# Performance work log

Measured on AMD Instinct MI355X. Metric: run time of the kernel, lower is better.

Reference implementation:

```python
import jax, jax.numpy as jnp
import numpy as np

B, T = 16384, 512          # batch, seq_len
DSTATE, DINPUT = 4, 4       # quaternion state / quaternion input
DMLP1, DMLP2 = 128, 128     # ODEFunc MLP hidden widths


def _linear_params(key, fan_in, fan_out):
    # torch nn.Linear default init: U(-1/sqrt(fan_in), 1/sqrt(fan_in))
    lim = 1.0 / np.sqrt(fan_in)
    kw, kb = jax.random.split(key)
    W = jax.random.uniform(kw, (fan_in, fan_out), jnp.float32, -lim, lim)
    b = jax.random.uniform(kb, (fan_out,), jnp.float32, -lim, lim)
    return W, b


def setup_inputs() -> dict:
    key = jax.random.key(0)
    k1, k2, k3, kx = jax.random.split(key, 4)
    W1, b1 = _linear_params(k1, DSTATE + DINPUT, DMLP1)
    W2, b2 = _linear_params(k2, DMLP1, DMLP2)
    W3, b3 = _linear_params(k3, DMLP2, DSTATE)
    quat_seq = jax.random.normal(kx, (B, T, DINPUT), jnp.float32)
    return {"quat_seq": quat_seq, "W1": W1, "b1": b1, "W2": W2, "b2": b2,
            "W3": W3, "b3": b3}


def reference(quat_seq, W1, b1, W2, b2, W3, b3):
    batch = quat_seq.shape[0]
    dstate = W3.shape[1]

    def odefunc(h, q):
        # f(t, [h, q]) -> dh/dt ; time is unused by the net
        x = jnp.concatenate([h, q], axis=-1)            # [B, DSTATE+DINPUT]
        x = jax.nn.silu(x @ W1 + b1)                    # [B, DMLP1]
        x = jax.nn.silu(x @ W2 + b2)                    # [B, DMLP2]
        return x @ W3 + b3                              # [B, DSTATE]

    dt = 1.0  # t_span = [0, 1] on a fixed grid -> single RK4 step of size 1

    def step(h, q_t):
        # torchdiffeq fixed-grid 'rk4' uses the 3/8-rule (rk4_alt_step_func)
        k1 = odefunc(h, q_t)
        k2 = odefunc(h + dt * k1 / 3.0, q_t)
        k3 = odefunc(h + dt * (k2 - k1 / 3.0), q_t)
        k4 = odefunc(h + dt * (k1 - k2 + k3), q_t)
        h_new = h + dt * (k1 + 3.0 * (k2 + k3) + k4) / 8.0
        return h_new, None

    h0 = jnp.zeros((batch, dstate), quat_seq.dtype).at[:, 0].set(1.0)
    # scan over time: [T, B, DINPUT]
    h_final, _ = jax.lax.scan(step, h0, jnp.swapaxes(quat_seq, 0, 1))
    return h_final
```

## Files before the change

kernel.cpp:

```cpp
#include <hip/hip_runtime.h>
#include <hip/hip_bf16.h>

typedef float f32x4 __attribute__((ext_vector_type(4)));
typedef short short8v __attribute__((ext_vector_type(8)));
typedef unsigned int uint;

constexpr int TSTEPS = 512;

union FragU { uint u[4]; short8v v; };

__device__ __forceinline__ float silu_f(float x) {
    return __fdividef(x, 1.0f + __expf(-x));
}

__device__ __forceinline__ uint bf16_rne(float x) {
    uint ux = __float_as_uint(x);
    return (ux + 0x7FFFu + ((ux >> 16) & 1u)) & 0xFFFF0000u;
}
__device__ __forceinline__ void split2u(float x, uint &h, uint &l) {
    h = bf16_rne(x);
    float rem = x - __uint_as_float(h);
    l = bf16_rne(rem);
}

__device__ __forceinline__ uint cvtpk(float a, float b) {
    union { __hip_bfloat162 h; uint u; } cv;
    cv.h = __float22bfloat162_rn(make_float2(a, b));
    return cv.u;
}
__device__ __forceinline__ void split4_pk(const f32x4 v, uint2 &hi, uint2 &lo) {
    hi.x = cvtpk(v.x, v.y);
    hi.y = cvtpk(v.z, v.w);
    float h0 = __uint_as_float(hi.x << 16);
    float h1 = __uint_as_float(hi.x & 0xFFFF0000u);
    float h2 = __uint_as_float(hi.y << 16);
    float h3 = __uint_as_float(hi.y & 0xFFFF0000u);
    lo.x = cvtpk(v.x - h0, v.y - h1);
    lo.y = cvtpk(v.z - h2, v.w - h3);
}

__device__ __forceinline__ f32x4 mfma4(const short8v *A, short8v Bh, short8v Bl,
                                       f32x4 c) {
    c = __builtin_amdgcn_mfma_f32_16x16x32_bf16(A[1], Bl, c, 0, 0, 0);
    c = __builtin_amdgcn_mfma_f32_16x16x32_bf16(A[1], Bh, c, 0, 0, 0);
    c = __builtin_amdgcn_mfma_f32_16x16x32_bf16(A[0], Bl, c, 0, 0, 0);
    c = __builtin_amdgcn_mfma_f32_16x16x32_bf16(A[0], Bh, c, 0, 0, 0);
    return c;
}

__global__ __launch_bounds__(256, 3)
void odernn_v7(const float* __restrict__ quat,
               const float* __restrict__ W1, const float* __restrict__ b1,
               const float* __restrict__ W2, const float* __restrict__ b2,
               const float* __restrict__ W3, const float* __restrict__ b3,
               float* __restrict__ out)
{
    __shared__ short sx1[2 * 16 * 16 * 8];
    __shared__ float sb1[128];
    __shared__ float sb2[128];
    __shared__ float sW3[128 * 4];
    __shared__ float sk3[4][16][4];

    const int tid  = threadIdx.x;
    const int w    = tid >> 6;
    const int lane = tid & 63;
    const int l15  = lane & 15;
    const int g    = lane >> 4;
    const int rowbase = blockIdx.x * 16;

    if (tid < 128) { sb1[tid] = b1[tid]; sb2[tid] = b2[tid]; }
    for (int i = tid; i < 512; i += 256) sW3[i] = W3[i];

    short8v A2[2][4][2];
#pragma unroll
    for (int mt = 0; mt < 2; ++mt) {
#pragma unroll
        for (int kt = 0; kt < 4; ++kt) {
#pragma unroll
            for (int e = 0; e < 8; ++e) {
                float x = W2[(32 * kt + 8 * g + e) * 128 + (32 * w + 16 * mt + l15)];
                uint h, l; split2u(x, h, l);
                A2[mt][kt][0][e] = (short)(h >> 16);
                A2[mt][kt][1][e] = (short)(l >> 16);
            }
        }
    }
    short8v A1[2];
#pragma unroll
    for (int mt = 0; mt < 2; ++mt) {
#pragma unroll
        for (int e = 0; e < 8; ++e) {
            float x = W1[e * 128 + (32 * w + 16 * mt + l15)];
            uint h, l; split2u(x, h, l);
            A1[mt][e] = (short)(((g < 2) ? h : l) >> 16);
        }
    }
    f32x4 b3v = *(const f32x4*)b3;

    __syncthreads();

    f32x4 h  = {1.0f, 0, 0, 0};
    f32x4 k1 = {0,0,0,0}, k2 = {0,0,0,0}, k3v = {0,0,0,0};
    const float* qp = quat + (size_t)(rowbase + l15) * TSTEPS * 4;

    const bool gsel = (g & 1);
    const int  half = (g & 1) * 4;
    const int  kc0  = 4 * w + (g >> 1);

#pragma unroll 1
    for (int t = 0; t < TSTEPS; ++t) {
        f32x4 q = *(const f32x4*)(qp + 4 * t);
        uint qs01, qs23;
        {
            uint2 qhi, qlo;
            split4_pk(q, qhi, qlo);
            qs01 = gsel ? qlo.x : qhi.x;
            qs23 = gsel ? qlo.y : qhi.y;
        }
        f32x4 hnew = {0,0,0,0};

#pragma unroll
        for (int s = 0; s < 4; ++s) {
            f32x4 hs = h;
            if (s == 1)      hs += k1 * (1.0f/3.0f);
            else if (s == 2) hs += k2 - k1 * (1.0f/3.0f);
            else if (s == 3) hs += k1 - k2 + k3v;

            FragU b0;
            {
                uint2 hhi, hlo;
                split4_pk(hs, hhi, hlo);
                b0.u[0] = gsel ? hlo.x : hhi.x;
                b0.u[1] = gsel ? hlo.y : hhi.y;
                b0.u[2] = qs01;
                b0.u[3] = qs23;
            }

            f32x4 c1_0 = *(const f32x4*)&sb1[32 * w + 4 * g];
            f32x4 c1_1 = *(const f32x4*)&sb1[32 * w + 16 + 4 * g];
            c1_0 = __builtin_amdgcn_mfma_f32_16x16x32_bf16(A1[0], b0.v, c1_0, 0, 0, 0);
            c1_1 = __builtin_amdgcn_mfma_f32_16x16x32_bf16(A1[1], b0.v, c1_1, 0, 0, 0);

#pragma unroll
            for (int mt = 0; mt < 2; ++mt) {
                const f32x4 c1 = mt ? c1_1 : c1_0;
                f32x4 sv;
#pragma unroll
                for (int r = 0; r < 4; ++r) sv[r] = silu_f(c1[r]);
                uint2 phi, plo;
                split4_pk(sv, phi, plo);
                const int kc = kc0 + 2 * mt;
                *(uint2*)&sx1[((0 * 16 + kc) * 16 + l15) * 8 + half] = phi;
                *(uint2*)&sx1[((1 * 16 + kc) * 16 + l15) * 8 + half] = plo;
            }
            __syncthreads();

            f32x4 u0 = *(const f32x4*)&sb2[32 * w + 4 * g],      v0 = {0,0,0,0};
            f32x4 u1 = *(const f32x4*)&sb2[32 * w + 16 + 4 * g], v1 = {0,0,0,0};
#pragma unroll
            for (int kt = 0; kt < 4; ++kt) {
                short8v Bh = *(const short8v*)&sx1[((0 * 16 + kt * 4 + g) * 16 + l15) * 8];
                short8v Bl = *(const short8v*)&sx1[((1 * 16 + kt * 4 + g) * 16 + l15) * 8];
                if (kt & 1) {
                    v0 = mfma4(A2[0][kt], Bh, Bl, v0);
                    v1 = mfma4(A2[1][kt], Bh, Bl, v1);
                } else {
                    u0 = mfma4(A2[0][kt], Bh, Bl, u0);
                    u1 = mfma4(A2[1][kt], Bh, Bl, u1);
                }
            }
            const f32x4 c20 = u0 + v0, c21 = u1 + v1;

            f32x4 p = {0,0,0,0};
#pragma unroll
            for (int mt = 0; mt < 2; ++mt) {
#pragma unroll
                for (int r = 0; r < 4; ++r) {
                    const int j = 32 * w + 16 * mt + 4 * g + r;
                    const float xv = silu_f(mt ? c21[r] : c20[r]);
                    p += xv * (*(const f32x4*)&sW3[j * 4]);
                }
            }
#pragma unroll
            for (int mx = 16; mx < 64; mx <<= 1) {
                p.x += __shfl_xor(p.x, mx, 64);
                p.y += __shfl_xor(p.y, mx, 64);
                p.z += __shfl_xor(p.z, mx, 64);
                p.w += __shfl_xor(p.w, mx, 64);
            }
            if (g == 0) *(f32x4*)&sk3[w][l15][0] = p;
            __syncthreads();

            f32x4 ks = b3v;
#pragma unroll
            for (int w2 = 0; w2 < 4; ++w2)
                ks += *(const f32x4*)&sk3[w2][l15][0];

            const float wgt = (s == 1 || s == 2) ? 0.375f : 0.125f;
            hnew += ks * wgt;
            if (s == 0)      k1  = ks;
            else if (s == 1) k2  = ks;
            else if (s == 2) k3v = ks;
        }
        h += hnew;
    }

    if (tid < 16)
        *(f32x4*)&out[(size_t)(rowbase + tid) * 4] = h;
}

extern "C" void kernel_launch(void* const* d_in, const int* in_sizes, int n_in,
                              void* d_out, int out_size, void* d_ws, size_t ws_size,
                              hipStream_t stream)
{
    const float* quat = (const float*)d_in[0];
    const float* W1   = (const float*)d_in[1];
    const float* b1   = (const float*)d_in[2];
    const float* W2   = (const float*)d_in[3];
    const float* b2   = (const float*)d_in[4];
    const float* W3   = (const float*)d_in[5];
    const float* b3   = (const float*)d_in[6];
    float* out        = (float*)d_out;

    const int B = in_sizes[0] / (TSTEPS * 4);
    dim3 grid(B / 16), block(256);
    hipLaunchKernelGGL(odernn_v7, grid, block, 0, stream,
                       quat, W1, b1, W2, b2, W3, b3, out);
}
```

Before: 7.830 ms.

## Switch to 32x32x16 MFMA tiles with 32 batch rows per block

Each block now handles 32 batch rows instead of 16 and uses 32x32x16 bf16 MFMAs in place of 16x16x32 ones for both MLP layers, with the shared-memory staging layout redone to match. This halves the grid and the per-row barrier and bias overhead, and puts more work into each MFMA issue. In exchange each block carries more accumulator registers, so launch bounds drop to 2 blocks per SM. The layer-1 split-bf16 trick becomes two MFMAs that swap the hi/lo halves.

Measured after the change: 7.385 ms. 5.7% less time.

```diff
diff --git a/kernel.cpp b/kernel.cpp
--- a/kernel.cpp
+++ b/kernel.cpp
@@ -1,7 +1,8 @@
 #include <hip/hip_runtime.h>
 #include <hip/hip_bf16.h>
 
-typedef float f32x4 __attribute__((ext_vector_type(4)));
+typedef float f32x4  __attribute__((ext_vector_type(4)));
+typedef float f32x16 __attribute__((ext_vector_type(16)));
 typedef short short8v __attribute__((ext_vector_type(8)));
 typedef unsigned int uint;
 
@@ -39,61 +40,48 @@
     lo.y = cvtpk(v.z - h2, v.w - h3);
 }
 
-__device__ __forceinline__ f32x4 mfma4(const short8v *A, short8v Bh, short8v Bl,
-                                       f32x4 c) {
-    c = __builtin_amdgcn_mfma_f32_16x16x32_bf16(A[1], Bl, c, 0, 0, 0);
-    c = __builtin_amdgcn_mfma_f32_16x16x32_bf16(A[1], Bh, c, 0, 0, 0);
-    c = __builtin_amdgcn_mfma_f32_16x16x32_bf16(A[0], Bl, c, 0, 0, 0);
-    c = __builtin_amdgcn_mfma_f32_16x16x32_bf16(A[0], Bh, c, 0, 0, 0);
-    return c;
-}
-
-__global__ __launch_bounds__(256, 3)
-void odernn_v7(const float* __restrict__ quat,
+#define SX1(lev,kt,gk,b) (((((lev)*8+(kt))*2+(gk))*32+(b))*8)
+
+__global__ __launch_bounds__(256, 2)
+void odernn_v8(const float* __restrict__ quat,
                const float* __restrict__ W1, const float* __restrict__ b1,
                const float* __restrict__ W2, const float* __restrict__ b2,
                const float* __restrict__ W3, const float* __restrict__ b3,
                float* __restrict__ out)
 {
-    __shared__ short sx1[2 * 16 * 16 * 8];
+    __shared__ short sx1[2 * 8 * 2 * 32 * 8];
     __shared__ float sb1[128];
     __shared__ float sb2[128];
-    __shared__ float sW3[128 * 4];
-    __shared__ float sk3[4][16][4];
+    __shared__ float sW3[512];
+    __shared__ float sk3[4][32][4];
 
     const int tid  = threadIdx.x;
     const int w    = tid >> 6;
     const int lane = tid & 63;
-    const int l15  = lane & 15;
-    const int g    = lane >> 4;
-    const int rowbase = blockIdx.x * 16;
+    const int b    = lane & 31;
+    const int gp   = lane >> 5;
+    const int rowbase = blockIdx.x * 32;
 
     if (tid < 128) { sb1[tid] = b1[tid]; sb2[tid] = b2[tid]; }
     for (int i = tid; i < 512; i += 256) sW3[i] = W3[i];
 
-    short8v A2[2][4][2];
-#pragma unroll
-    for (int mt = 0; mt < 2; ++mt) {
-#pragma unroll
-        for (int kt = 0; kt < 4; ++kt) {
-#pragma unroll
-            for (int e = 0; e < 8; ++e) {
-                float x = W2[(32 * kt + 8 * g + e) * 128 + (32 * w + 16 * mt + l15)];
-                uint h, l; split2u(x, h, l);
-                A2[mt][kt][0][e] = (short)(h >> 16);
-                A2[mt][kt][1][e] = (short)(l >> 16);
-            }
+    short8v A2[8][2];
+#pragma unroll
+    for (int kt = 0; kt < 8; ++kt) {
+#pragma unroll
+        for (int e = 0; e < 8; ++e) {
+            float x = W2[(16 * kt + 8 * gp + e) * 128 + (32 * w + b)];
+            uint h, l; split2u(x, h, l);
+            A2[kt][0][e] = (short)(h >> 16);
+            A2[kt][1][e] = (short)(l >> 16);
         }
     }
-    short8v A1[2];
-#pragma unroll
-    for (int mt = 0; mt < 2; ++mt) {
-#pragma unroll
-        for (int e = 0; e < 8; ++e) {
-            float x = W1[e * 128 + (32 * w + 16 * mt + l15)];
-            uint h, l; split2u(x, h, l);
-            A1[mt][e] = (short)(((g < 2) ? h : l) >> 16);
-        }
+    short8v A1;
+#pragma unroll
+    for (int e = 0; e < 8; ++e) {
+        float x = W1[e * 128 + (32 * w + b)];
+        uint h, l; split2u(x, h, l);
+        A1[e] = (short)((gp ? l : h) >> 16);
     }
     f32x4 b3v = *(const f32x4*)b3;
 
@@ -101,22 +89,13 @@
 
     f32x4 h  = {1.0f, 0, 0, 0};
     f32x4 k1 = {0,0,0,0}, k2 = {0,0,0,0}, k3v = {0,0,0,0};
-    const float* qp = quat + (size_t)(rowbase + l15) * TSTEPS * 4;
-
-    const bool gsel = (g & 1);
-    const int  half = (g & 1) * 4;
-    const int  kc0  = 4 * w + (g >> 1);
+    const float* qp = quat + (size_t)(rowbase + b) * TSTEPS * 4;
 
 #pragma unroll 1
     for (int t = 0; t < TSTEPS; ++t) {
         f32x4 q = *(const f32x4*)(qp + 4 * t);
-        uint qs01, qs23;
-        {
-            uint2 qhi, qlo;
-            split4_pk(q, qhi, qlo);
-            qs01 = gsel ? qlo.x : qhi.x;
-            qs23 = gsel ? qlo.y : qhi.y;
-        }
+        uint2 qhi, qlo;
+        split4_pk(q, qhi, qlo);
         f32x4 hnew = {0,0,0,0};
 
 #pragma unroll
@@ -126,75 +105,73 @@
             else if (s == 2) hs += k2 - k1 * (1.0f/3.0f);
             else if (s == 3) hs += k1 - k2 + k3v;
 
-            FragU b0;
-            {
-                uint2 hhi, hlo;
-                split4_pk(hs, hhi, hlo);
-                b0.u[0] = gsel ? hlo.x : hhi.x;
-                b0.u[1] = gsel ? hlo.y : hhi.y;
-                b0.u[2] = qs01;
-                b0.u[3] = qs23;
-            }
-
-            f32x4 c1_0 = *(const f32x4*)&sb1[32 * w + 4 * g];
-            f32x4 c1_1 = *(const f32x4*)&sb1[32 * w + 16 + 4 * g];
-            c1_0 = __builtin_amdgcn_mfma_f32_16x16x32_bf16(A1[0], b0.v, c1_0, 0, 0, 0);
-            c1_1 = __builtin_amdgcn_mfma_f32_16x16x32_bf16(A1[1], b0.v, c1_1, 0, 0, 0);
-
-#pragma unroll
-            for (int mt = 0; mt < 2; ++mt) {
-                const f32x4 c1 = mt ? c1_1 : c1_0;
+            uint2 hhi, hlo;
+            split4_pk(hs, hhi, hlo);
+            FragU b0a, b0b;
+            b0a.u[0] = gp ? hlo.x : hhi.x;  b0a.u[1] = gp ? hlo.y : hhi.y;
+            b0a.u[2] = gp ? qlo.x : qhi.x;  b0a.u[3] = gp ? qlo.y : qhi.y;
+            b0b.u[0] = gp ? hhi.x : hlo.x;  b0b.u[1] = gp ? hhi.y : hlo.y;
+            b0b.u[2] = gp ? qhi.x : qlo.x;  b0b.u[3] = gp ? qhi.y : qlo.y;
+
+            f32x16 c1;
+#pragma unroll
+            for (int qd = 0; qd < 4; ++qd) {
+                f32x4 bv = *(const f32x4*)&sb1[32 * w + 8 * qd + 4 * gp];
+                c1[4*qd+0] = bv.x; c1[4*qd+1] = bv.y;
+                c1[4*qd+2] = bv.z; c1[4*qd+3] = bv.w;
+            }
+            c1 = __builtin_amdgcn_mfma_f32_32x32x16_bf16(A1, b0a.v, c1, 0, 0, 0);
+            c1 = __builtin_amdgcn_mfma_f32_32x32x16_bf16(A1, b0b.v, c1, 0, 0, 0);
+
+#pragma unroll
+            for (int qd = 0; qd < 4; ++qd) {
                 f32x4 sv;
-#pragma unroll
-                for (int r = 0; r < 4; ++r) sv[r] = silu_f(c1[r]);
+                sv.x = silu_f(c1[4*qd+0]); sv.y = silu_f(c1[4*qd+1]);
+                sv.z = silu_f(c1[4*qd+2]); sv.w = silu_f(c1[4*qd+3]);
                 uint2 phi, plo;
                 split4_pk(sv, phi, plo);
-                const int kc = kc0 + 2 * mt;
-                *(uint2*)&sx1[((0 * 16 + kc) * 16 + l15) * 8 + half] = phi;
-                *(uint2*)&sx1[((1 * 16 + kc) * 16 + l15) * 8 + half] = plo;
+                const int kt = 2 * w + (qd >> 1);
+                const int gk = qd & 1;
+                *(uint2*)&sx1[SX1(0, kt, gk, b) + 4 * gp] = phi;
+                *(uint2*)&sx1[SX1(1, kt, gk, b) + 4 * gp] = plo;
             }
             __syncthreads();
 
-            f32x4 u0 = *(const f32x4*)&sb2[32 * w + 4 * g],      v0 = {0,0,0,0};
-            f32x4 u1 = *(const f32x4*)&sb2[32 * w + 16 + 4 * g], v1 = {0,0,0,0};
-#pragma unroll
-            for (int kt = 0; kt < 4; ++kt) {
-                short8v Bh = *(const short8v*)&sx1[((0 * 16 + kt * 4 + g) * 16 + l15) * 8];
-                short8v Bl = *(const short8v*)&sx1[((1 * 16 + kt * 4 + g) * 16 + l15) * 8];
-                if (kt & 1) {
-                    v0 = mfma4(A2[0][kt], Bh, Bl, v0);
-                    v1 = mfma4(A2[1][kt], Bh, Bl, v1);
-                } else {
-                    u0 = mfma4(A2[0][kt], Bh, Bl, u0);
-                    u1 = mfma4(A2[1][kt], Bh, Bl, u1);
-                }
-            }
-            const f32x4 c20 = u0 + v0, c21 = u1 + v1;
+            f32x16 c2;
+#pragma unroll
+            for (int qd = 0; qd < 4; ++qd) {
+                f32x4 bv = *(const f32x4*)&sb2[32 * w + 8 * qd + 4 * gp];
+                c2[4*qd+0] = bv.x; c2[4*qd+1] = bv.y;
+                c2[4*qd+2] = bv.z; c2[4*qd+3] = bv.w;
+            }
+#pragma unroll
+            for (int kt = 0; kt < 8; ++kt) {
+                short8v Bh = *(const short8v*)&sx1[SX1(0, kt, gp, b)];
+                short8v Bl = *(const short8v*)&sx1[SX1(1, kt, gp, b)];
+                c2 = __builtin_amdgcn_mfma_f32_32x32x16_bf16(A2[kt][1], Bl, c2, 0, 0, 0);
+                c2 = __builtin_amdgcn_mfma_f32_32x32x16_bf16(A2[kt][1], Bh, c2, 0, 0, 0);
+                c2 = __builtin_amdgcn_mfma_f32_32x32x16_bf16(A2[kt][0], Bl, c2, 0, 0, 0);
+                c2 = __builtin_amdgcn_mfma_f32_32x32x16_bf16(A2[kt][0], Bh, c2, 0, 0, 0);
+            }
 
             f32x4 p = {0,0,0,0};
 #pragma unroll
-            for (int mt = 0; mt < 2; ++mt) {
-#pragma unroll
-                for (int r = 0; r < 4; ++r) {
-                    const int j = 32 * w + 16 * mt + 4 * g + r;
-                    const float xv = silu_f(mt ? c21[r] : c20[r]);
-                    p += xv * (*(const f32x4*)&sW3[j * 4]);
-                }
-            }
-#pragma unroll
-            for (int mx = 16; mx < 64; mx <<= 1) {
-                p.x += __shfl_xor(p.x, mx, 64);
-                p.y += __shfl_xor(p.y, mx, 64);
-                p.z += __shfl_xor(p.z, mx, 64);
-                p.w += __shfl_xor(p.w, mx, 64);
-            }
-            if (g == 0) *(f32x4*)&sk3[w][l15][0] = p;
+            for (int i = 0; i < 16; ++i) {
+                const int j = 32 * w + 8 * (i >> 2) + (i & 3) + 4 * gp;
+                const float xv = silu_f(c2[i]);
+                p += xv * (*(const f32x4*)&sW3[j * 4]);
+            }
+            p.x += __shfl_xor(p.x, 32, 64);
+            p.y += __shfl_xor(p.y, 32, 64);
+            p.z += __shfl_xor(p.z, 32, 64);
+            p.w += __shfl_xor(p.w, 32, 64);
+            if (lane < 32) *(f32x4*)&sk3[w][lane][0] = p;
             __syncthreads();
 
             f32x4 ks = b3v;
 #pragma unroll
             for (int w2 = 0; w2 < 4; ++w2)
-                ks += *(const f32x4*)&sk3[w2][l15][0];
+                ks += *(const f32x4*)&sk3[w2][b][0];
 
             const float wgt = (s == 1 || s == 2) ? 0.375f : 0.125f;
             hnew += ks * wgt;
@@ -205,7 +182,7 @@
         h += hnew;
     }
 
-    if (tid < 16)
+    if (tid < 32)
         *(f32x4*)&out[(size_t)(rowbase + tid) * 4] = h;
 }
 
@@ -223,7 +200,7 @@
     float* out        = (float*)d_out;
 
     const int B = in_sizes[0] / (TSTEPS * 4);
-    dim3 grid(B / 16), block(256);
-    hipLaunchKernelGGL(odernn_v7, grid, block, 0, stream,
+    dim3 grid(B / 32), block(256);
+    hipLaunchKernelGGL(odernn_v8, grid, block, 0, stream,
                        quat, W1, b1, W2, b2, W3, b3, out);
 }
```

## Run each 16-row tile in a single wavefront, removing block barriers

Applied to the files above, without the earlier changes.

Each 16-row batch tile now runs in one 64-thread wavefront instead of four waves. The wave keeps all of W2 (hi/lo bf16 split) in registers, folds b1 into the layer-1 MFMA through a constant-one input lane, and computes layer 3 with MFMAs instead of a shuffle reduction. This removes the per-stage __syncthreads and the cross-wave reduction, drops one of the four bf16 split products in layer 2, and prefetches the next quaternion. In exchange it puts a large register footprint on each wave and gives up intra-block parallelism, so latency hiding depends on having enough resident blocks.

Result: slower. 9.457 ms (+20.8%).

```diff
diff --git a/kernel.cpp b/kernel.cpp
--- a/kernel.cpp
+++ b/kernel.cpp
@@ -11,6 +11,12 @@
 
 __device__ __forceinline__ float silu_f(float x) {
     return __fdividef(x, 1.0f + __expf(-x));
+}
+__device__ __forceinline__ f32x4 silu4(f32x4 v) {
+    f32x4 r;
+    r.x = silu_f(v.x); r.y = silu_f(v.y);
+    r.z = silu_f(v.z); r.w = silu_f(v.w);
+    return r;
 }
 
 __device__ __forceinline__ uint bf16_rne(float x) {
@@ -22,7 +28,6 @@
     float rem = x - __uint_as_float(h);
     l = bf16_rne(rem);
 }
-
 __device__ __forceinline__ uint cvtpk(float a, float b) {
     union { __hip_bfloat162 h; uint u; } cv;
     cv.h = __float22bfloat162_rn(make_float2(a, b));
@@ -39,84 +44,85 @@
     lo.y = cvtpk(v.z - h2, v.w - h3);
 }
 
-__device__ __forceinline__ f32x4 mfma4(const short8v *A, short8v Bh, short8v Bl,
-                                       f32x4 c) {
-    c = __builtin_amdgcn_mfma_f32_16x16x32_bf16(A[1], Bl, c, 0, 0, 0);
-    c = __builtin_amdgcn_mfma_f32_16x16x32_bf16(A[1], Bh, c, 0, 0, 0);
-    c = __builtin_amdgcn_mfma_f32_16x16x32_bf16(A[0], Bl, c, 0, 0, 0);
-    c = __builtin_amdgcn_mfma_f32_16x16x32_bf16(A[0], Bh, c, 0, 0, 0);
-    return c;
-}
-
-__global__ __launch_bounds__(256, 3)
-void odernn_v7(const float* __restrict__ quat,
-               const float* __restrict__ W1, const float* __restrict__ b1,
-               const float* __restrict__ W2, const float* __restrict__ b2,
-               const float* __restrict__ W3, const float* __restrict__ b3,
-               float* __restrict__ out)
+#define MFMA16(A, B, C) __builtin_amdgcn_mfma_f32_16x16x32_bf16((A), (B), (C), 0, 0, 0)
+
+#define SXI(lev, p, bb) ((((lev)*16 + (p))*16 + (bb))*8)
+
+__global__ __launch_bounds__(64, 1)
+void odernn_v11(const float* __restrict__ quat,
+                const float* __restrict__ W1, const float* __restrict__ b1,
+                const float* __restrict__ W2, const float* __restrict__ b2,
+                const float* __restrict__ W3, const float* __restrict__ b3,
+                float* __restrict__ out)
 {
     __shared__ short sx1[2 * 16 * 16 * 8];
-    __shared__ float sb1[128];
-    __shared__ float sb2[128];
-    __shared__ float sW3[128 * 4];
-    __shared__ float sk3[4][16][4];
-
-    const int tid  = threadIdx.x;
-    const int w    = tid >> 6;
-    const int lane = tid & 63;
-    const int l15  = lane & 15;
-    const int g    = lane >> 4;
+    __shared__ short sx2[2 * 16 * 16 * 8];
+    __shared__ float sb2s[128];
+    __shared__ float sck[64];
+
+    const int tid = threadIdx.x;
+    const int b   = tid & 15;
+    const int g   = tid >> 4;
     const int rowbase = blockIdx.x * 16;
 
-    if (tid < 128) { sb1[tid] = b1[tid]; sb2[tid] = b2[tid]; }
-    for (int i = tid; i < 512; i += 256) sW3[i] = W3[i];
-
-    short8v A2[2][4][2];
-#pragma unroll
-    for (int mt = 0; mt < 2; ++mt) {
-#pragma unroll
-        for (int kt = 0; kt < 4; ++kt) {
+    sb2s[tid]      = b2[tid];
+    sb2s[tid + 64] = b2[tid + 64];
+
+    short8v A2[8][4][2];
+#pragma unroll
+    for (int jt = 0; jt < 8; ++jt)
+#pragma unroll
+        for (int kt = 0; kt < 4; ++kt)
 #pragma unroll
             for (int e = 0; e < 8; ++e) {
-                float x = W2[(32 * kt + 8 * g + e) * 128 + (32 * w + 16 * mt + l15)];
-                uint h, l; split2u(x, h, l);
-                A2[mt][kt][0][e] = (short)(h >> 16);
-                A2[mt][kt][1][e] = (short)(l >> 16);
-            }
+                uint h_, l_;
+                split2u(W2[(32*kt + 8*g + e) * 128 + (16*jt + b)], h_, l_);
+                A2[jt][kt][0][e] = (short)(h_ >> 16);
+                A2[jt][kt][1][e] = (short)(l_ >> 16);
+            }
+
+    short8v A1[8];
+#pragma unroll
+    for (int jt = 0; jt < 8; ++jt)
+#pragma unroll
+        for (int e = 0; e < 8; ++e) {
+            short val;
+            if (g == 3) {
+                uint h_, l_; split2u(b1[16*jt + b], h_, l_);
+                val = (e == 0) ? (short)(h_ >> 16) : (e == 1) ? (short)(l_ >> 16) : (short)0;
+            } else {
+                uint h_, l_; split2u(W1[e * 128 + 16*jt + b], h_, l_);
+                val = (short)(((g == 2) ? l_ : h_) >> 16);
+            }
+            A1[jt][e] = val;
         }
-    }
-    short8v A1[2];
-#pragma unroll
-    for (int mt = 0; mt < 2; ++mt) {
+
+    short8v A3[4][2];
+#pragma unroll
+    for (int kt = 0; kt < 4; ++kt)
 #pragma unroll
         for (int e = 0; e < 8; ++e) {
-            float x = W1[e * 128 + (32 * w + 16 * mt + l15)];
-            uint h, l; split2u(x, h, l);
-            A1[mt][e] = (short)(((g < 2) ? h : l) >> 16);
+            float x = (b < 4) ? W3[(32*kt + 8*g + e) * 4 + b] : 0.0f;
+            uint h_, l_; split2u(x, h_, l_);
+            A3[kt][0][e] = (short)(h_ >> 16);
+            A3[kt][1][e] = (short)(l_ >> 16);
         }
-    }
+
     f32x4 b3v = *(const f32x4*)b3;
 
     __syncthreads();
 
-    f32x4 h  = {1.0f, 0, 0, 0};
+    f32x4 h  = {1.0f, 0.0f, 0.0f, 0.0f};
     f32x4 k1 = {0,0,0,0}, k2 = {0,0,0,0}, k3v = {0,0,0,0};
-    const float* qp = quat + (size_t)(rowbase + l15) * TSTEPS * 4;
-
-    const bool gsel = (g & 1);
-    const int  half = (g & 1) * 4;
-    const int  kc0  = 4 * w + (g >> 1);
+    const float* qp = quat + (size_t)(rowbase + b) * TSTEPS * 4;
+    f32x4 qnext = *(const f32x4*)qp;
 
 #pragma unroll 1
     for (int t = 0; t < TSTEPS; ++t) {
-        f32x4 q = *(const f32x4*)(qp + 4 * t);
-        uint qs01, qs23;
-        {
-            uint2 qhi, qlo;
-            split4_pk(q, qhi, qlo);
-            qs01 = gsel ? qlo.x : qhi.x;
-            qs23 = gsel ? qlo.y : qhi.y;
-        }
+        const f32x4 q = qnext;
+        const int tn = (t + 1 < TSTEPS) ? t + 1 : t;
+        qnext = *(const f32x4*)(qp + 4 * tn);
+        uint2 qhi, qlo; split4_pk(q, qhi, qlo);
         f32x4 hnew = {0,0,0,0};
 
 #pragma unroll
@@ -126,75 +132,77 @@
             else if (s == 2) hs += k2 - k1 * (1.0f/3.0f);
             else if (s == 3) hs += k1 - k2 + k3v;
 
+            uint2 hhi, hlo; split4_pk(hs, hhi, hlo);
             FragU b0;
-            {
-                uint2 hhi, hlo;
-                split4_pk(hs, hhi, hlo);
-                b0.u[0] = gsel ? hlo.x : hhi.x;
-                b0.u[1] = gsel ? hlo.y : hhi.y;
-                b0.u[2] = qs01;
-                b0.u[3] = qs23;
-            }
-
-            f32x4 c1_0 = *(const f32x4*)&sb1[32 * w + 4 * g];
-            f32x4 c1_1 = *(const f32x4*)&sb1[32 * w + 16 + 4 * g];
-            c1_0 = __builtin_amdgcn_mfma_f32_16x16x32_bf16(A1[0], b0.v, c1_0, 0, 0, 0);
-            c1_1 = __builtin_amdgcn_mfma_f32_16x16x32_bf16(A1[1], b0.v, c1_1, 0, 0, 0);
-
-#pragma unroll
-            for (int mt = 0; mt < 2; ++mt) {
-                const f32x4 c1 = mt ? c1_1 : c1_0;
-                f32x4 sv;
-#pragma unroll
-                for (int r = 0; r < 4; ++r) sv[r] = silu_f(c1[r]);
-                uint2 phi, plo;
-                split4_pk(sv, phi, plo);
-                const int kc = kc0 + 2 * mt;
-                *(uint2*)&sx1[((0 * 16 + kc) * 16 + l15) * 8 + half] = phi;
-                *(uint2*)&sx1[((1 * 16 + kc) * 16 + l15) * 8 + half] = plo;
-            }
-            __syncthreads();
-
-            f32x4 u0 = *(const f32x4*)&sb2[32 * w + 4 * g],      v0 = {0,0,0,0};
-            f32x4 u1 = *(const f32x4*)&sb2[32 * w + 16 + 4 * g], v1 = {0,0,0,0};
+            if (g == 3)      { b0.u[0] = 0x3F803F80u; b0.u[1] = 0u; b0.u[2] = 0u; b0.u[3] = 0u; }
+            else if (g == 1) { b0.u[0] = hlo.x; b0.u[1] = hlo.y; b0.u[2] = qlo.x; b0.u[3] = qlo.y; }
+            else             { b0.u[0] = hhi.x; b0.u[1] = hhi.y; b0.u[2] = qhi.x; b0.u[3] = qhi.y; }
+
+#pragma unroll
+            for (int jt = 0; jt < 8; ++jt) {
+                f32x4 z = {0,0,0,0};
+                f32x4 c1 = MFMA16(A1[jt], b0.v, z);
+                f32x4 sv = silu4(c1);
+                uint2 phi, plo; split4_pk(sv, phi, plo);
+                const int c  = 4*jt + g;
+                const int p  = c >> 1;
+                const int hf = (c & 1) * 4;
+                *(uint2*)&sx1[SXI(0, p, b) + hf] = phi;
+                *(uint2*)&sx1[SXI(1, p, b) + hf] = plo;
+            }
+
+            short8v B2[4][2];
 #pragma unroll
             for (int kt = 0; kt < 4; ++kt) {
-                short8v Bh = *(const short8v*)&sx1[((0 * 16 + kt * 4 + g) * 16 + l15) * 8];
-                short8v Bl = *(const short8v*)&sx1[((1 * 16 + kt * 4 + g) * 16 + l15) * 8];
+                B2[kt][0] = *(const short8v*)&sx1[SXI(0, 4*kt + g, b)];
+                B2[kt][1] = *(const short8v*)&sx1[SXI(1, 4*kt + g, b)];
+            }
+
+#pragma unroll
+            for (int jt = 0; jt < 8; ++jt) {
+                f32x4 u = {0,0,0,0}, vv = {0,0,0,0};
+#pragma unroll
+                for (int kt = 0; kt < 4; ++kt) {
+                    if (kt & 1) {
+                        vv = MFMA16(A2[jt][kt][1], B2[kt][0], vv);
+                        vv = MFMA16(A2[jt][kt][0], B2[kt][1], vv);
+                        vv = MFMA16(A2[jt][kt][0], B2[kt][0], vv);
+                    } else {
+                        u  = MFMA16(A2[jt][kt][1], B2[kt][0], u);
+                        u  = MFMA16(A2[jt][kt][0], B2[kt][1], u);
+                        u  = MFMA16(A2[jt][kt][0], B2[kt][0], u);
+                    }
+                }
+                f32x4 bb = *(const f32x4*)&sb2s[16*jt + 4*g];
+                f32x4 xv = silu4(u + vv + bb);
+                uint2 phi, plo; split4_pk(xv, phi, plo);
+                const int c  = 4*jt + g;
+                const int p  = c >> 1;
+                const int hf = (c & 1) * 4;
+                *(uint2*)&sx2[SXI(0, p, b) + hf] = phi;
+                *(uint2*)&sx2[SXI(1, p, b) + hf] = plo;
+            }
+
+            f32x4 c3a = {0,0,0,0}, c3b = {0,0,0,0};
+#pragma unroll
+            for (int kt = 0; kt < 4; ++kt) {
+                short8v Bh = *(const short8v*)&sx2[SXI(0, 4*kt + g, b)];
+                short8v Bl = *(const short8v*)&sx2[SXI(1, 4*kt + g, b)];
                 if (kt & 1) {
-                    v0 = mfma4(A2[0][kt], Bh, Bl, v0);
-                    v1 = mfma4(A2[1][kt], Bh, Bl, v1);
+                    c3b = MFMA16(A3[kt][1], Bl, c3b);
+                    c3b = MFMA16(A3[kt][1], Bh, c3b);
+                    c3b = MFMA16(A3[kt][0], Bl, c3b);
+                    c3b = MFMA16(A3[kt][0], Bh, c3b);
                 } else {
-                    u0 = mfma4(A2[0][kt], Bh, Bl, u0);
-                    u1 = mfma4(A2[1][kt], Bh, Bl, u1);
+                    c3a = MFMA16(A3[kt][1], Bl, c3a);
+                    c3a = MFMA16(A3[kt][1], Bh, c3a);
+                    c3a = MFMA16(A3[kt][0], Bl, c3a);
+                    c3a = MFMA16(A3[kt][0], Bh, c3a);
                 }
             }
-            const f32x4 c20 = u0 + v0, c21 = u1 + v1;
-
-            f32x4 p = {0,0,0,0};
-#pragma unroll
-            for (int mt = 0; mt < 2; ++mt) {
-#pragma unroll
-                for (int r = 0; r < 4; ++r) {
-                    const int j = 32 * w + 16 * mt + 4 * g + r;
-                    const float xv = silu_f(mt ? c21[r] : c20[r]);
-                    p += xv * (*(const f32x4*)&sW3[j * 4]);
-                }
-            }
-#pragma unroll
-            for (int mx = 16; mx < 64; mx <<= 1) {
-                p.x += __shfl_xor(p.x, mx, 64);
-                p.y += __shfl_xor(p.y, mx, 64);
-                p.z += __shfl_xor(p.z, mx, 64);
-                p.w += __shfl_xor(p.w, mx, 64);
-            }
-            if (g == 0) *(f32x4*)&sk3[w][l15][0] = p;
-            __syncthreads();
-
-            f32x4 ks = b3v;
-#pragma unroll
-            for (int w2 = 0; w2 < 4; ++w2)
-                ks += *(const f32x4*)&sk3[w2][l15][0];
+            f32x4 c3 = c3a + c3b;
+            if (tid < 16) *(f32x4*)&sck[b * 4] = c3;
+            f32x4 ks = *(const f32x4*)&sck[b * 4] + b3v;
 
             const float wgt = (s == 1 || s == 2) ? 0.375f : 0.125f;
             hnew += ks * wgt;
@@ -206,7 +214,7 @@
     }
 
     if (tid < 16)
-        *(f32x4*)&out[(size_t)(rowbase + tid) * 4] = h;
+        *(f32x4*)&out[(size_t)(rowbase + b) * 4] = h;
 }
 
 extern "C" void kernel_launch(void* const* d_in, const int* in_sizes, int n_in,
@@ -223,7 +231,7 @@
     float* out        = (float*)d_out;
 
     const int B = in_sizes[0] / (TSTEPS * 4);
-    dim3 grid(B / 16), block(256);
-    hipLaunchKernelGGL(odernn_v7, grid, block, 0, stream,
+    dim3 grid(B / 16), block(64);
+    hipLaunchKernelGGL(odernn_v11, grid, block, 0, stream,
                        quat, W1, b1, W2, b2, W3, b3, out);
 }
```
